# Kernel optimization log

Measured on AMD Instinct MI355X. Metric: run time of the kernel, lower is better.

The kernel has to match this reference:

```python
import jax, jax.numpy as jnp
import numpy as np

N_ATOMS, E_ATOMS, E_BONDS, N_FRAGS, E_FRAGS = 200000, 800000, 3200000, 20000, 60000
D, EB, H, DH = 128, 12, 3, 4  # atom dim, bond-node feat dim, n_heads, per-head dim (EB // H)


def _seg_softmax(logits, seg, num):
    # scatter_softmax over segments given by `seg` along axis 0
    m = jax.ops.segment_max(logits, seg, num_segments=num)
    m = jnp.where(jnp.isfinite(m), m, 0.0)  # guard empty segments
    e = jnp.exp(logits - m[seg])
    s = jax.ops.segment_sum(e, seg, num_segments=num)
    return e / s[seg]


def setup_inputs() -> dict:
    key = jax.random.key(0)
    ks = jax.random.split(key, 16)
    s = 0.05
    return dict(
        x_atoms=jax.random.normal(ks[0], (N_ATOMS, D), jnp.float32),
        edge_index=jax.random.randint(ks[1], (2, E_ATOMS), 0, N_ATOMS, jnp.int32),
        edge_attr=jax.random.normal(ks[2], (E_ATOMS, EB), jnp.float32),
        frag_index=jax.random.randint(ks[3], (2, E_FRAGS), 0, N_FRAGS, jnp.int32),
        x_frags=jax.random.normal(ks[4], (N_FRAGS, D), jnp.float32),
        atom_to_frag_ids=jax.random.randint(ks[5], (N_ATOMS,), 0, N_FRAGS, jnp.int32),
        node_features_bond_graph=jax.random.normal(ks[6], (E_ATOMS, EB), jnp.float32),
        edge_index_bonds_graph=jax.random.randint(ks[7], (2, E_BONDS), 0, E_ATOMS, jnp.int32),
        edge_attr_bond_graph=jax.random.normal(ks[8], (E_BONDS, 1), jnp.float32),
        W_atom=jax.random.normal(ks[9], (D, D), jnp.float32) * s,
        b_atom=jnp.zeros((D,), jnp.float32),
        W_edge=jax.random.normal(ks[10], (EB, D), jnp.float32) * s,
        b_edge=jnp.zeros((D,), jnp.float32),
        W_proj=jax.random.normal(ks[11], (EB, EB), jnp.float32) * s,
        b_proj=jnp.zeros((EB,), jnp.float32),
        a_b=jax.random.normal(ks[12], (H, 2 * DH + 1), jnp.float32) * s,
        W_f1=jax.random.normal(ks[13], (D, 2 * D), jnp.float32) * s,
        b_f1=jnp.zeros((2 * D,), jnp.float32),
        W_f2=jax.random.normal(ks[14], (2 * D, D), jnp.float32) * s,
        b_f2=jnp.zeros((D,), jnp.float32),
    )


def reference(x_atoms, edge_index, edge_attr, frag_index, x_frags, atom_to_frag_ids,
              node_features_bond_graph, edge_index_bonds_graph, edge_attr_bond_graph,
              W_atom, b_atom, W_edge, b_edge, W_proj, b_proj, a_b,
              W_f1, b_f1, W_f2, b_f2):
    Nb = node_features_bond_graph.shape[0]  # bond-graph nodes == atom-graph edges
    N = x_atoms.shape[0]
    Nf = x_frags.shape[0]

    # ---- GAT-style attention on the bond (line) graph ----
    tgt_b, src_b = edge_index_bonds_graph[0], edge_index_bonds_graph[1]
    nf = (node_features_bond_graph @ W_proj + b_proj).reshape(Nb, H, DH)
    tf = nf[tgt_b]                                  # [Eb, H, DH]
    sf = nf[src_b]                                  # [Eb, H, DH]
    ea = jnp.broadcast_to(edge_attr_bond_graph[:, None, :], (tgt_b.shape[0], H, 1))
    msg = jnp.concatenate([tf, ea, sf], axis=-1)    # [Eb, H, 2*DH+1]
    logits = jax.nn.leaky_relu(jnp.sum(msg * a_b, axis=2), 0.2)  # [Eb, H]
    attn = _seg_softmax(logits, tgt_b, Nb)
    agg = jax.ops.segment_sum(attn[..., None] * sf, tgt_b, num_segments=Nb)  # [Nb, H, DH]
    new_bond = agg.reshape(Nb, H * DH)              # [Nb, EB]

    # edge embedding (computed in the original forward; not used in returned outputs)
    edge_attr_full = jnp.concatenate(
        [new_bond, jnp.zeros((N, EB), edge_attr.dtype)], axis=0)
    _ = edge_attr_full @ W_edge + b_edge

    # ---- degree-normalized GCN propagation on atom graph with self loops ----
    x = x_atoms @ W_atom + b_atom
    loop = jnp.arange(N, dtype=edge_index.dtype)
    src = jnp.concatenate([edge_index[0], loop])
    tgt = jnp.concatenate([edge_index[1], loop])
    deg = jax.ops.segment_sum(jnp.ones(src.shape, x.dtype), src, num_segments=N)
    dinv = jnp.where(deg > 0, 1.0 / jnp.sqrt(jnp.maximum(deg, 1.0)), 0.0)
    norm = dinv[src] * dinv[tgt]
    x_new = jax.ops.segment_sum(x[src] * norm[:, None], tgt, num_segments=N)  # [N, D]

    # ---- fragment pooling + fragment-graph propagation ----
    frag_feat = jax.ops.segment_sum(x_new, atom_to_frag_ids, num_segments=Nf)  # [Nf, D]
    fs, ft = frag_index[0], frag_index[1]
    frag_sum = jax.ops.segment_sum(frag_feat[fs], ft, num_segments=Nf)
    frag_out = jax.nn.relu(frag_sum @ W_f1 + b_f1) @ W_f2 + b_f2
    return (x_new, frag_out)
```

## Files before the change

### kernel.cpp

```cpp
#include <hip/hip_runtime.h>
#include <hip/hip_bf16.h>
#include <cstddef>

#define NA 200000
#define EA 800000
#define NF 20000
#define EF 60000
#define TOTW (EA + NA + EF)
#define CAPE 32
#define CAPA 64
#define CAPF 32

typedef unsigned short ushort_t;
typedef __attribute__((ext_vector_type(8))) short bf16x8;
typedef __attribute__((ext_vector_type(4))) float f32x4;

__device__ __forceinline__ unsigned short f2bf(float f) {
  unsigned u = __builtin_bit_cast(unsigned, f);
  u += 0x7FFFu + ((u >> 16) & 1u);
  return (unsigned short)(u >> 16);
}
__device__ __forceinline__ float bf2f(unsigned short h) {
  unsigned u = ((unsigned)h) << 16;
  return __builtin_bit_cast(float, u);
}
__device__ __forceinline__ void acc2(float& a, float& b, unsigned v) {
  a += __builtin_bit_cast(float, v << 16);
  b += __builtin_bit_cast(float, v & 0xFFFF0000u);
}

__global__ __launch_bounds__(256) void k_build(
    const int* __restrict__ ei, const int* __restrict__ a2f,
    const int* __restrict__ fi, int* __restrict__ cnt_src,
    int* __restrict__ cnt_e, int* __restrict__ cnt_a, int* __restrict__ cnt_f,
    int* __restrict__ lst_e, int* __restrict__ lst_a, int* __restrict__ lst_f) {
  int idx = blockIdx.x * 256 + threadIdx.x;
  if (idx < EA) {
    int s = ei[idx], t = ei[EA + idx];
    atomicAdd(&cnt_src[s], 1);
    int p = atomicAdd(&cnt_e[t], 1);
    if (p < CAPE) lst_e[t * CAPE + p] = s;
  } else if (idx < EA + NA) {
    int i = idx - EA;
    int f = a2f[i];
    int p = atomicAdd(&cnt_a[f], 1);
    if (p < CAPA) lst_a[f * CAPA + p] = i;
  } else if (idx < TOTW) {
    int e = idx - EA - NA;
    int p = atomicAdd(&cnt_f[fi[EF + e]], 1);
    if (p < CAPF) lst_f[fi[EF + e] * CAPF + p] = fi[e];
  }
}

__global__ __launch_bounds__(256) void k_wt(const float* __restrict__ W,
                                            ushort_t* __restrict__ Wt) {
  int idx = blockIdx.x * 256 + threadIdx.x;
  if (idx < 128 * 128) {
    int c = idx >> 7, k = idx & 127;
    Wt[idx] = f2bf(W[k * 128 + c]);
  }
}

__global__ __launch_bounds__(256) void k_gemm_y(
    const float* __restrict__ xa, const ushort_t* __restrict__ Wt,
    const float* __restrict__ b, const int* __restrict__ cnt_src,
    ushort_t* __restrict__ y) {
  __shared__ ushort_t Asl[64 * 128];
  __shared__ ushort_t Bsl[128 * 128];
  const int tid = threadIdx.x;
  const int brow = blockIdx.x * 64;
  {
    const float4* gA = reinterpret_cast<const float4*>(xa + (size_t)brow * 128);
#pragma unroll
    for (int i = 0; i < 8; ++i) {
      int f = tid + i * 256;
      int row = f >> 5;
      int kq = f & 31;
      float4 v = gA[f];
      ushort4 u;
      u.x = f2bf(v.x); u.y = f2bf(v.y); u.z = f2bf(v.z); u.w = f2bf(v.w);
      int koff = (kq * 4) ^ ((row & 7) << 3);
      *reinterpret_cast<ushort4*>(&Asl[row * 128 + koff]) = u;
    }
    const uint4* gW = reinterpret_cast<const uint4*>(Wt);
#pragma unroll
    for (int i = 0; i < 8; ++i) {
      int u = tid + i * 256;
      int c = u >> 4;
      int k8 = u & 15;
      uint4 v = gW[u];
      int koff = (k8 * 8) ^ ((c & 7) << 3);
      *reinterpret_cast<uint4*>(&Bsl[c * 128 + koff]) = v;
    }
  }
  __syncthreads();
  const int w = tid >> 6;
  const int l = tid & 63;
  const int lr = l & 15;
  const int g = l >> 4;
  const int r0 = w * 16;
  f32x4 acc[8] = {};
  const int arow = r0 + lr;
  const int asw = (arow & 7) << 3;
#pragma unroll
  for (int s = 0; s < 4; ++s) {
    const int kb = s * 32 + g * 4;
    ushort4 alo = *reinterpret_cast<const ushort4*>(&Asl[arow * 128 + (kb ^ asw)]);
    ushort4 ahi = *reinterpret_cast<const ushort4*>(&Asl[arow * 128 + ((kb + 16) ^ asw)]);
    bf16x8 a;
    a[0] = (short)alo.x; a[1] = (short)alo.y; a[2] = (short)alo.z; a[3] = (short)alo.w;
    a[4] = (short)ahi.x; a[5] = (short)ahi.y; a[6] = (short)ahi.z; a[7] = (short)ahi.w;
#pragma unroll
    for (int t = 0; t < 8; ++t) {
      const int bc = t * 16 + lr;
      const int bsw = (bc & 7) << 3;
      ushort4 blo = *reinterpret_cast<const ushort4*>(&Bsl[bc * 128 + (kb ^ bsw)]);
      ushort4 bhi = *reinterpret_cast<const ushort4*>(&Bsl[bc * 128 + ((kb + 16) ^ bsw)]);
      bf16x8 bf;
      bf[0] = (short)blo.x; bf[1] = (short)blo.y; bf[2] = (short)blo.z; bf[3] = (short)blo.w;
      bf[4] = (short)bhi.x; bf[5] = (short)bhi.y; bf[6] = (short)bhi.z; bf[7] = (short)bhi.w;
      acc[t] = __builtin_amdgcn_mfma_f32_16x16x32_bf16(a, bf, acc[t], 0, 0, 0);
    }
  }
  float di[4];
#pragma unroll
  for (int r = 0; r < 4; ++r)
    di[r] = rsqrtf(1.0f + (float)cnt_src[brow + r0 + g * 4 + r]);
#pragma unroll
  for (int t = 0; t < 8; ++t) {
    const int col = t * 16 + lr;
    const float bb = b[col];
#pragma unroll
    for (int r = 0; r < 4; ++r) {
      const int row = brow + r0 + g * 4 + r;
      y[(size_t)row * 128 + col] = f2bf((acc[t][r] + bb) * di[r]);
    }
  }
}

__global__ __launch_bounds__(256) void k_gather_x(
    const int* __restrict__ cnt_e, const int* __restrict__ lst_e,
    const ushort_t* __restrict__ y, const int* __restrict__ cnt_src,
    float* __restrict__ xnew) {
  const int row = blockIdx.x * 16 + (threadIdx.x >> 4);
  const int lane = threadIdx.x & 15;
  const int c0 = lane * 8;
  float a0, a1, a2, a3, a4, a5, a6, a7;
  {
    uint4 v = *reinterpret_cast<const uint4*>(y + (size_t)row * 128 + c0);
    a0 = __builtin_bit_cast(float, v.x << 16);
    a1 = __builtin_bit_cast(float, v.x & 0xFFFF0000u);
    a2 = __builtin_bit_cast(float, v.y << 16);
    a3 = __builtin_bit_cast(float, v.y & 0xFFFF0000u);
    a4 = __builtin_bit_cast(float, v.z << 16);
    a5 = __builtin_bit_cast(float, v.z & 0xFFFF0000u);
    a6 = __builtin_bit_cast(float, v.w << 16);
    a7 = __builtin_bit_cast(float, v.w & 0xFFFF0000u);
  }
  const int base = row * CAPE;
  int deg = cnt_e[row];
  deg = (deg < CAPE) ? deg : CAPE;
  int j = 0;
  for (; j + 4 <= deg; j += 4) {
    const int s0 = lst_e[base + j + 0];
    const int s1 = lst_e[base + j + 1];
    const int s2 = lst_e[base + j + 2];
    const int s3 = lst_e[base + j + 3];
    const uint4 w0 = *reinterpret_cast<const uint4*>(y + (size_t)s0 * 128 + c0);
    const uint4 w1 = *reinterpret_cast<const uint4*>(y + (size_t)s1 * 128 + c0);
    const uint4 w2 = *reinterpret_cast<const uint4*>(y + (size_t)s2 * 128 + c0);
    const uint4 w3 = *reinterpret_cast<const uint4*>(y + (size_t)s3 * 128 + c0);
    acc2(a0, a1, w0.x); acc2(a2, a3, w0.y); acc2(a4, a5, w0.z); acc2(a6, a7, w0.w);
    acc2(a0, a1, w1.x); acc2(a2, a3, w1.y); acc2(a4, a5, w1.z); acc2(a6, a7, w1.w);
    acc2(a0, a1, w2.x); acc2(a2, a3, w2.y); acc2(a4, a5, w2.z); acc2(a6, a7, w2.w);
    acc2(a0, a1, w3.x); acc2(a2, a3, w3.y); acc2(a4, a5, w3.z); acc2(a6, a7, w3.w);
  }
  for (; j < deg; ++j) {
    const int s = lst_e[base + j];
    const uint4 w = *reinterpret_cast<const uint4*>(y + (size_t)s * 128 + c0);
    acc2(a0, a1, w.x); acc2(a2, a3, w.y); acc2(a4, a5, w.z); acc2(a6, a7, w.w);
  }
  const float dt = rsqrtf(1.0f + (float)cnt_src[row]);
  f32x4 q0 = {a0 * dt, a1 * dt, a2 * dt, a3 * dt};
  f32x4 q1 = {a4 * dt, a5 * dt, a6 * dt, a7 * dt};
  float* o = xnew + (size_t)row * 128 + c0;
  __builtin_nontemporal_store(q0, reinterpret_cast<f32x4*>(o));
  __builtin_nontemporal_store(q1, reinterpret_cast<f32x4*>(o + 4));
}

__global__ __launch_bounds__(256) void k_gather_ff(
    const int* __restrict__ cnt_a, const int* __restrict__ lst_a,
    const float* __restrict__ xnew, float* __restrict__ ff) {
  const int f = blockIdx.x * 8 + (threadIdx.x >> 5);
  const int c = (threadIdx.x & 31) << 2;
  float4 acc = {0.f, 0.f, 0.f, 0.f};
  const int base = f * CAPA;
  int deg = cnt_a[f];
  deg = (deg < CAPA) ? deg : CAPA;
  int j = 0;
  for (; j + 4 <= deg; j += 4) {
    const int s0 = lst_a[base + j + 0];
    const int s1 = lst_a[base + j + 1];
    const int s2 = lst_a[base + j + 2];
    const int s3 = lst_a[base + j + 3];
    const float4 v0 = *reinterpret_cast<const float4*>(xnew + (size_t)s0 * 128 + c);
    const float4 v1 = *reinterpret_cast<const float4*>(xnew + (size_t)s1 * 128 + c);
    const float4 v2 = *reinterpret_cast<const float4*>(xnew + (size_t)s2 * 128 + c);
    const float4 v3 = *reinterpret_cast<const float4*>(xnew + (size_t)s3 * 128 + c);
    acc.x += v0.x + v1.x + v2.x + v3.x;
    acc.y += v0.y + v1.y + v2.y + v3.y;
    acc.z += v0.z + v1.z + v2.z + v3.z;
    acc.w += v0.w + v1.w + v2.w + v3.w;
  }
  for (; j < deg; ++j) {
    const int s = lst_a[base + j];
    const float4 v = *reinterpret_cast<const float4*>(xnew + (size_t)s * 128 + c);
    acc.x += v.x; acc.y += v.y; acc.z += v.z; acc.w += v.w;
  }
  *reinterpret_cast<float4*>(ff + (size_t)f * 128 + c) = acc;
}

__global__ __launch_bounds__(256) void k_mlp(
    const int* __restrict__ cnt_f, const int* __restrict__ lst_f,
    const float* __restrict__ ff,
    const float* __restrict__ W1, const float* __restrict__ b1,
    const float* __restrict__ W2, const float* __restrict__ b2,
    float* __restrict__ out) {
  __shared__ float As[32][128];
  __shared__ float hs[32][256];
  const int row0 = blockIdx.x * 32;
  {
    const int g = threadIdx.x >> 5;
    const int c = (threadIdx.x & 31) << 2;
#pragma unroll
    for (int rr = 0; rr < 4; ++rr) {
      const int f = row0 + g * 4 + rr;
      const int base = f * CAPF;
      int deg = cnt_f[f];
      deg = (deg < CAPF) ? deg : CAPF;
      float4 acc = {0.f, 0.f, 0.f, 0.f};
      for (int j = 0; j < deg; ++j) {
        const int s = lst_f[base + j];
        const float4 v = *reinterpret_cast<const float4*>(ff + (size_t)s * 128 + c);
        acc.x += v.x; acc.y += v.y; acc.z += v.z; acc.w += v.w;
      }
      *reinterpret_cast<float4*>(&As[g * 4 + rr][c]) = acc;
    }
  }
  __syncthreads();
  {
    const int tc = threadIdx.x & 63;
    const int tr = threadIdx.x >> 6;
    const int c0 = tc * 4;
    float acc[8][4] = {};
    for (int k0 = 0; k0 < 128; k0 += 4) {
      float4 w0 = *reinterpret_cast<const float4*>(&W1[(k0 + 0) * 256 + c0]);
      float4 w1 = *reinterpret_cast<const float4*>(&W1[(k0 + 1) * 256 + c0]);
      float4 w2 = *reinterpret_cast<const float4*>(&W1[(k0 + 2) * 256 + c0]);
      float4 w3 = *reinterpret_cast<const float4*>(&W1[(k0 + 3) * 256 + c0]);
#pragma unroll
      for (int r = 0; r < 8; ++r) {
        float4 a = *reinterpret_cast<const float4*>(&As[tr * 8 + r][k0]);
        acc[r][0] += a.x * w0.x + a.y * w1.x + a.z * w2.x + a.w * w3.x;
        acc[r][1] += a.x * w0.y + a.y * w1.y + a.z * w2.y + a.w * w3.y;
        acc[r][2] += a.x * w0.z + a.y * w1.z + a.z * w2.z + a.w * w3.z;
        acc[r][3] += a.x * w0.w + a.y * w1.w + a.z * w2.w + a.w * w3.w;
      }
    }
    const float4 bc = *reinterpret_cast<const float4*>(&b1[c0]);
#pragma unroll
    for (int r = 0; r < 8; ++r) {
      float4 h;
      h.x = fmaxf(acc[r][0] + bc.x, 0.f);
      h.y = fmaxf(acc[r][1] + bc.y, 0.f);
      h.z = fmaxf(acc[r][2] + bc.z, 0.f);
      h.w = fmaxf(acc[r][3] + bc.w, 0.f);
      *reinterpret_cast<float4*>(&hs[tr * 8 + r][c0]) = h;
    }
  }
  __syncthreads();
  {
    const int tc = threadIdx.x & 31;
    const int tr = threadIdx.x >> 5;
    const int c0 = tc * 4;
    float acc[4][4] = {};
    for (int k0 = 0; k0 < 256; k0 += 4) {
      float4 w0 = *reinterpret_cast<const float4*>(&W2[(k0 + 0) * 128 + c0]);
      float4 w1 = *reinterpret_cast<const float4*>(&W2[(k0 + 1) * 128 + c0]);
      float4 w2 = *reinterpret_cast<const float4*>(&W2[(k0 + 2) * 128 + c0]);
      float4 w3 = *reinterpret_cast<const float4*>(&W2[(k0 + 3) * 128 + c0]);
#pragma unroll
      for (int r = 0; r < 4; ++r) {
        float4 a = *reinterpret_cast<const float4*>(&hs[tr * 4 + r][k0]);
        acc[r][0] += a.x * w0.x + a.y * w1.x + a.z * w2.x + a.w * w3.x;
        acc[r][1] += a.x * w0.y + a.y * w1.y + a.z * w2.y + a.w * w3.y;
        acc[r][2] += a.x * w0.z + a.y * w1.z + a.z * w2.z + a.w * w3.z;
        acc[r][3] += a.x * w0.w + a.y * w1.w + a.z * w2.w + a.w * w3.w;
      }
    }
    const float4 bc = *reinterpret_cast<const float4*>(&b2[c0]);
#pragma unroll
    for (int r = 0; r < 4; ++r) {
      float4 o;
      o.x = acc[r][0] + bc.x;
      o.y = acc[r][1] + bc.y;
      o.z = acc[r][2] + bc.z;
      o.w = acc[r][3] + bc.w;
      *reinterpret_cast<float4*>(&out[(size_t)(row0 + tr * 4 + r) * 128 + c0]) = o;
    }
  }
}

extern "C" void kernel_launch(void* const* d_in, const int* in_sizes, int n_in,
                              void* d_out, int out_size, void* d_ws, size_t ws_size,
                              hipStream_t stream) {
  const float* x_atoms    = (const float*)d_in[0];
  const int*   edge_index = (const int*)d_in[1];
  const int*   frag_index = (const int*)d_in[3];
  const int*   a2f        = (const int*)d_in[5];
  const float* W_atom     = (const float*)d_in[9];
  const float* b_atom     = (const float*)d_in[10];
  const float* W_f1       = (const float*)d_in[16];
  const float* b_f1       = (const float*)d_in[17];
  const float* W_f2       = (const float*)d_in[18];
  const float* b_f2       = (const float*)d_in[19];

  char* ws = (char*)d_ws;
  size_t off = 0;
  auto alloc = [&](size_t bytes) {
    void* p = ws + off;
    off += (bytes + 255) & ~(size_t)255;
    return p;
  };
  int* cnt_src = (int*)alloc((size_t)NA * 4);
  int* cnt_e   = (int*)alloc((size_t)NA * 4);
  int* cnt_a   = (int*)alloc((size_t)NF * 4);
  int* cnt_f   = (int*)alloc((size_t)NF * 4);
  const size_t zero_bytes = off;
  int* lst_e   = (int*)alloc((size_t)NA * CAPE * 4);
  int* lst_a   = (int*)alloc((size_t)NF * CAPA * 4);
  int* lst_f   = (int*)alloc((size_t)NF * CAPF * 4);
  ushort_t* Wt = (ushort_t*)alloc((size_t)128 * 128 * 2);
  ushort_t* y  = (ushort_t*)alloc((size_t)NA * 128 * 2);
  float* ff    = (float*)alloc((size_t)NF * 128 * 4);

  float* xnew = (float*)d_out;
  float* fout = (float*)d_out + (size_t)NA * 128;

  (void)hipMemsetAsync(ws, 0, zero_bytes, stream);

  k_build<<<(TOTW + 255) / 256, 256, 0, stream>>>(edge_index, a2f, frag_index,
                                                  cnt_src, cnt_e, cnt_a, cnt_f,
                                                  lst_e, lst_a, lst_f);
  k_wt<<<64, 256, 0, stream>>>(W_atom, Wt);
  k_gemm_y  <<<NA / 64, 256, 0, stream>>>(x_atoms, Wt, b_atom, cnt_src, y);
  k_gather_x<<<NA / 16, 256, 0, stream>>>(cnt_e, lst_e, y, cnt_src, xnew);
  k_gather_ff<<<NF / 8, 256, 0, stream>>>(cnt_a, lst_a, xnew, ff);
  k_mlp     <<<NF / 32, 256, 0, stream>>>(cnt_f, lst_f, ff, W_f1, b_f1,
                                          W_f2, b_f2, fout);
}
```

Measured before the change: 277.4 us.

## Fuse adjacency build into GEMM kernel and move degree scaling into gather

The separate adjacency-building kernel is merged into the front of the GEMM kernel as a grid-stride loop, so the atomics and list writes can overlap with the bf16 MFMA transform of atom features. To remove the GEMM's dependency on final source degrees, y is now stored unscaled. The gather kernel instead applies each neighbour's inverse-sqrt degree per edge via FMA. This adds a random cnt_src load and an rsqrt per neighbour in the gather, and the fused kernel's GEMM blocks now wait on atomic-heavy work.

Measured after the change: 267.6 us. 1.04x faster.

```diff
diff --git a/kernel.cpp b/kernel.cpp
--- a/kernel.cpp
+++ b/kernel.cpp
@@ -10,6 +10,7 @@
 #define CAPE 32
 #define CAPA 64
 #define CAPF 32
+#define GRIDY (NA / 64)
 
 typedef unsigned short ushort_t;
 typedef __attribute__((ext_vector_type(8))) short bf16x8;
@@ -20,36 +21,9 @@
   u += 0x7FFFu + ((u >> 16) & 1u);
   return (unsigned short)(u >> 16);
 }
-__device__ __forceinline__ float bf2f(unsigned short h) {
-  unsigned u = ((unsigned)h) << 16;
-  return __builtin_bit_cast(float, u);
-}
-__device__ __forceinline__ void acc2(float& a, float& b, unsigned v) {
-  a += __builtin_bit_cast(float, v << 16);
-  b += __builtin_bit_cast(float, v & 0xFFFF0000u);
-}
-
-__global__ __launch_bounds__(256) void k_build(
-    const int* __restrict__ ei, const int* __restrict__ a2f,
-    const int* __restrict__ fi, int* __restrict__ cnt_src,
-    int* __restrict__ cnt_e, int* __restrict__ cnt_a, int* __restrict__ cnt_f,
-    int* __restrict__ lst_e, int* __restrict__ lst_a, int* __restrict__ lst_f) {
-  int idx = blockIdx.x * 256 + threadIdx.x;
-  if (idx < EA) {
-    int s = ei[idx], t = ei[EA + idx];
-    atomicAdd(&cnt_src[s], 1);
-    int p = atomicAdd(&cnt_e[t], 1);
-    if (p < CAPE) lst_e[t * CAPE + p] = s;
-  } else if (idx < EA + NA) {
-    int i = idx - EA;
-    int f = a2f[i];
-    int p = atomicAdd(&cnt_a[f], 1);
-    if (p < CAPA) lst_a[f * CAPA + p] = i;
-  } else if (idx < TOTW) {
-    int e = idx - EA - NA;
-    int p = atomicAdd(&cnt_f[fi[EF + e]], 1);
-    if (p < CAPF) lst_f[fi[EF + e] * CAPF + p] = fi[e];
-  }
+__device__ __forceinline__ void acc2s(float& a, float& b, unsigned v, float s) {
+  a = fmaf(__builtin_bit_cast(float, v << 16), s, a);
+  b = fmaf(__builtin_bit_cast(float, v & 0xFFFF0000u), s, b);
 }
 
 __global__ __launch_bounds__(256) void k_wt(const float* __restrict__ W,
@@ -61,14 +35,36 @@
   }
 }
 
-__global__ __launch_bounds__(256) void k_gemm_y(
+__global__ __launch_bounds__(256) void k_fused(
+    const int* __restrict__ ei, const int* __restrict__ a2f,
+    const int* __restrict__ fi, int* __restrict__ cnt_src,
+    int* __restrict__ cnt_e, int* __restrict__ cnt_a, int* __restrict__ cnt_f,
+    int* __restrict__ lst_e, int* __restrict__ lst_a, int* __restrict__ lst_f,
     const float* __restrict__ xa, const ushort_t* __restrict__ Wt,
-    const float* __restrict__ b, const int* __restrict__ cnt_src,
-    ushort_t* __restrict__ y) {
+    const float* __restrict__ b, ushort_t* __restrict__ y) {
   __shared__ ushort_t Asl[64 * 128];
   __shared__ ushort_t Bsl[128 * 128];
   const int tid = threadIdx.x;
   const int brow = blockIdx.x * 64;
+
+  for (int idx = blockIdx.x * 256 + tid; idx < TOTW; idx += GRIDY * 256) {
+    if (idx < EA) {
+      int s = ei[idx], t = ei[EA + idx];
+      atomicAdd(&cnt_src[s], 1);
+      int p = atomicAdd(&cnt_e[t], 1);
+      if (p < CAPE) lst_e[t * CAPE + p] = s;
+    } else if (idx < EA + NA) {
+      int i = idx - EA;
+      int f = a2f[i];
+      int p = atomicAdd(&cnt_a[f], 1);
+      if (p < CAPA) lst_a[f * CAPA + p] = i;
+    } else {
+      int e = idx - EA - NA;
+      int p = atomicAdd(&cnt_f[fi[EF + e]], 1);
+      if (p < CAPF) lst_f[fi[EF + e] * CAPF + p] = fi[e];
+    }
+  }
+
   {
     const float4* gA = reinterpret_cast<const float4*>(xa + (size_t)brow * 128);
 #pragma unroll
@@ -122,10 +118,6 @@
       acc[t] = __builtin_amdgcn_mfma_f32_16x16x32_bf16(a, bf, acc[t], 0, 0, 0);
     }
   }
-  float di[4];
-#pragma unroll
-  for (int r = 0; r < 4; ++r)
-    di[r] = rsqrtf(1.0f + (float)cnt_src[brow + r0 + g * 4 + r]);
 #pragma unroll
   for (int t = 0; t < 8; ++t) {
     const int col = t * 16 + lr;
@@ -133,7 +125,7 @@
 #pragma unroll
     for (int r = 0; r < 4; ++r) {
       const int row = brow + r0 + g * 4 + r;
-      y[(size_t)row * 128 + col] = f2bf((acc[t][r] + bb) * di[r]);
+      y[(size_t)row * 128 + col] = f2bf(acc[t][r] + bb);
     }
   }
 }
@@ -145,17 +137,12 @@
   const int row = blockIdx.x * 16 + (threadIdx.x >> 4);
   const int lane = threadIdx.x & 15;
   const int c0 = lane * 8;
-  float a0, a1, a2, a3, a4, a5, a6, a7;
+  const float dt = rsqrtf(1.0f + (float)cnt_src[row]);
+  float a0 = 0, a1 = 0, a2 = 0, a3 = 0, a4 = 0, a5 = 0, a6 = 0, a7 = 0;
   {
     uint4 v = *reinterpret_cast<const uint4*>(y + (size_t)row * 128 + c0);
-    a0 = __builtin_bit_cast(float, v.x << 16);
-    a1 = __builtin_bit_cast(float, v.x & 0xFFFF0000u);
-    a2 = __builtin_bit_cast(float, v.y << 16);
-    a3 = __builtin_bit_cast(float, v.y & 0xFFFF0000u);
-    a4 = __builtin_bit_cast(float, v.z << 16);
-    a5 = __builtin_bit_cast(float, v.z & 0xFFFF0000u);
-    a6 = __builtin_bit_cast(float, v.w << 16);
-    a7 = __builtin_bit_cast(float, v.w & 0xFFFF0000u);
+    acc2s(a0, a1, v.x, dt); acc2s(a2, a3, v.y, dt);
+    acc2s(a4, a5, v.z, dt); acc2s(a6, a7, v.w, dt);
   }
   const int base = row * CAPE;
   int deg = cnt_e[row];
@@ -166,21 +153,26 @@
     const int s1 = lst_e[base + j + 1];
     const int s2 = lst_e[base + j + 2];
     const int s3 = lst_e[base + j + 3];
+    const float d0 = rsqrtf(1.0f + (float)cnt_src[s0]);
+    const float d1 = rsqrtf(1.0f + (float)cnt_src[s1]);
+    const float d2 = rsqrtf(1.0f + (float)cnt_src[s2]);
+    const float d3 = rsqrtf(1.0f + (float)cnt_src[s3]);
     const uint4 w0 = *reinterpret_cast<const uint4*>(y + (size_t)s0 * 128 + c0);
     const uint4 w1 = *reinterpret_cast<const uint4*>(y + (size_t)s1 * 128 + c0);
     const uint4 w2 = *reinterpret_cast<const uint4*>(y + (size_t)s2 * 128 + c0);
     const uint4 w3 = *reinterpret_cast<const uint4*>(y + (size_t)s3 * 128 + c0);
-    acc2(a0, a1, w0.x); acc2(a2, a3, w0.y); acc2(a4, a5, w0.z); acc2(a6, a7, w0.w);
-    acc2(a0, a1, w1.x); acc2(a2, a3, w1.y); acc2(a4, a5, w1.z); acc2(a6, a7, w1.w);
-    acc2(a0, a1, w2.x); acc2(a2, a3, w2.y); acc2(a4, a5, w2.z); acc2(a6, a7, w2.w);
-    acc2(a0, a1, w3.x); acc2(a2, a3, w3.y); acc2(a4, a5, w3.z); acc2(a6, a7, w3.w);
+    acc2s(a0, a1, w0.x, d0); acc2s(a2, a3, w0.y, d0); acc2s(a4, a5, w0.z, d0); acc2s(a6, a7, w0.w, d0);
+    acc2s(a0, a1, w1.x, d1); acc2s(a2, a3, w1.y, d1); acc2s(a4, a5, w1.z, d1); acc2s(a6, a7, w1.w, d1);
+    acc2s(a0, a1, w2.x, d2); acc2s(a2, a3, w2.y, d2); acc2s(a4, a5, w2.z, d2); acc2s(a6, a7, w2.w, d2);
+    acc2s(a0, a1, w3.x, d3); acc2s(a2, a3, w3.y, d3); acc2s(a4, a5, w3.z, d3); acc2s(a6, a7, w3.w, d3);
   }
   for (; j < deg; ++j) {
     const int s = lst_e[base + j];
+    const float dn = rsqrtf(1.0f + (float)cnt_src[s]);
     const uint4 w = *reinterpret_cast<const uint4*>(y + (size_t)s * 128 + c0);
-    acc2(a0, a1, w.x); acc2(a2, a3, w.y); acc2(a4, a5, w.z); acc2(a6, a7, w.w);
-  }
-  const float dt = rsqrtf(1.0f + (float)cnt_src[row]);
+    acc2s(a0, a1, w.x, dn); acc2s(a2, a3, w.y, dn);
+    acc2s(a4, a5, w.z, dn); acc2s(a6, a7, w.w, dn);
+  }
   f32x4 q0 = {a0 * dt, a1 * dt, a2 * dt, a3 * dt};
   f32x4 q1 = {a4 * dt, a5 * dt, a6 * dt, a7 * dt};
   float* o = xnew + (size_t)row * 128 + c0;
@@ -349,11 +341,11 @@
 
   (void)hipMemsetAsync(ws, 0, zero_bytes, stream);
 
-  k_build<<<(TOTW + 255) / 256, 256, 0, stream>>>(edge_index, a2f, frag_index,
-                                                  cnt_src, cnt_e, cnt_a, cnt_f,
-                                                  lst_e, lst_a, lst_f);
   k_wt<<<64, 256, 0, stream>>>(W_atom, Wt);
-  k_gemm_y  <<<NA / 64, 256, 0, stream>>>(x_atoms, Wt, b_atom, cnt_src, y);
+  k_fused<<<GRIDY, 256, 0, stream>>>(edge_index, a2f, frag_index,
+                                     cnt_src, cnt_e, cnt_a, cnt_f,
+                                     lst_e, lst_a, lst_f,
+                                     x_atoms, Wt, b_atom, y);
   k_gather_x<<<NA / 16, 256, 0, stream>>>(cnt_e, lst_e, y, cnt_src, xnew);
   k_gather_ff<<<NF / 8, 256, 0, stream>>>(cnt_a, lst_a, xnew, ff);
   k_mlp     <<<NF / 32, 256, 0, stream>>>(cnt_f, lst_f, ff, W_f1, b_f1,
```
